# Optimization experiments

Measured on AMD Instinct MI355X. Metric: run time of the kernel, lower is better.

## Reference

```python
import jax, jax.numpy as jnp
import numpy as np
import math

# ---- module hyperparameters (from init_kwargs) ----
IN_CHANS, OUT_CHANS = 64, 64
NLAT_IN, NLON_IN = 91, 180
NLAT_OUT, NLON_OUT = 91, 180  # same resolution -> longitudinal stride 1
NR, NPHI = 5, 6               # kernel_shape
KSIZE = (NR - 1) * NPHI + 1   # 25 basis functions (1 center + (NR-1)*NPHI ring sectors)
THETA_CUTOFF = 4.0 * math.pi / float(NLAT_OUT - 1)
# latitude support window: basis vanishes for |theta_out - theta_in| > cutoff
_HALF = int(math.ceil(THETA_CUTOFF / (math.pi / (NLAT_IN - 1))))
WIN = 2 * _HALF + 1


def _precompute_psi():
    """Precompute DISCO basis tensor psi (values of the piecewise-linear
    spherical basis functions, weighted by quadrature weights), restricted to
    the latitudinal support window. Returns (psi [K,To,W,P], ti_idx [To,W])."""
    theta_in = np.pi * np.arange(NLAT_IN) / (NLAT_IN - 1)    # equiangular colatitudes
    theta_out = np.pi * np.arange(NLAT_OUT) / (NLAT_OUT - 1)
    phi_in = 2.0 * np.pi * np.arange(NLON_IN) / NLON_IN
    offs = np.arange(-_HALF, _HALF + 1)
    ti_raw = np.arange(NLAT_OUT)[:, None] + offs[None, :]    # [To, W]
    valid = (ti_raw >= 0) & (ti_raw < NLAT_IN)
    ti_idx = np.clip(ti_raw, 0, NLAT_IN - 1)
    to = theta_out[:, None, None]                            # [To,1,1]
    ti = theta_in[ti_idx][:, :, None]                        # [To,W,1]
    ph = phi_in[None, None, :]                               # [1,1,P]
    # coordinates of input point in frame where the output point (theta_out, 0)
    # is rotated to the north pole (rotation by -theta_out about y-axis)
    xx = np.cos(to) * np.sin(ti) * np.cos(ph) - np.sin(to) * np.cos(ti)
    yy = np.sin(ti) * np.sin(ph)
    zz = np.sin(to) * np.sin(ti) * np.cos(ph) + np.cos(to) * np.cos(ti)
    r = np.arccos(np.clip(zz, -1.0, 1.0))                    # great-circle distance
    phi = np.mod(np.arctan2(yy, xx), 2.0 * np.pi)            # azimuth around output point
    dr = THETA_CUTOFF / (NR - 1)
    dphi = 2.0 * np.pi / NPHI
    inside = (r <= THETA_CUTOFF) & valid[:, :, None]
    psi = np.zeros((KSIZE,) + r.shape, dtype=np.float64)
    # k = 0: isotropic center hat
    psi[0] = np.where(inside, np.maximum(0.0, 1.0 - r / dr), 0.0)
    # rings ir = 1..NR-1, azimuthal sectors ip = 0..NPHI-1 (periodic hat in phi)
    for ir in range(1, NR):
        rad = np.maximum(0.0, 1.0 - np.abs(r - ir * dr) / dr)
        for ip in range(NPHI):
            dp = np.abs(np.mod(phi - ip * dphi + np.pi, 2.0 * np.pi) - np.pi)
            ang = np.maximum(0.0, 1.0 - dp / dphi)
            psi[1 + (ir - 1) * NPHI + ip] = np.where(inside, rad * ang, 0.0)
    # fold in equiangular quadrature weights of the input grid
    quad = np.sin(theta_in) * (np.pi / (NLAT_IN - 1)) * (2.0 * np.pi / NLON_IN)
    psi = psi * quad[ti_idx][None, :, :, None]
    return jnp.asarray(psi, dtype=jnp.float32), jnp.asarray(ti_idx, dtype=jnp.int32)


PSI, TI_IDX = _precompute_psi()  # PSI: [K, To, W, P], TI_IDX: [To, W]


def setup_inputs() -> dict:
    key = jax.random.key(0)
    k1, k2 = jax.random.split(key)
    x = jax.random.normal(k1, (2, IN_CHANS, NLAT_IN, NLON_IN), dtype=jnp.float32)
    scale = 1.0 / math.sqrt(IN_CHANS * KSIZE)
    weight = scale * jax.random.normal(k2, (OUT_CHANS, IN_CHANS, KSIZE), dtype=jnp.float32)
    return {"x": x, "weight": weight}


def reference(x, weight):
    # DISCO S2 conv: out[b,o,to,q] = sum_{c,k} w[o,c,k] * sum_{ti,p} psi[k,to,ti,(p-q) mod P] * x[b,c,ti,p]
    # The longitudinal shift is a circular cross-correlation -> evaluate via rFFT.
    x = x.astype(jnp.float32)  # wrapper casts to float32 around the conv
    xw = x[:, :, TI_IDX, :]                          # [B,C,To,W,P] latitudinal gather
    Xf = jnp.fft.rfft(xw, axis=-1)                   # [B,C,To,W,F]
    Pf = jnp.fft.rfft(PSI, axis=-1)                  # [K,To,W,F]
    # correlation: FFT(z) = conj(FFT(psi)) * FFT(x), contracting the lat window
    Zf = jnp.einsum('ktwf,bctwf->bcktf', jnp.conj(Pf), Xf)   # [B,C,K,To,F]
    Of = jnp.einsum('ock,bcktf->botf', weight.astype(Zf.dtype), Zf)
    out = jnp.fft.irfft(Of, n=NLON_IN, axis=-1)      # [B,Cout,To,P]
    return out.astype(x.dtype)
```

## Files before the change

### kernel.cpp

```cpp
#include <hip/hip_runtime.h>
#include <math.h>
#include <string.h>

#define NLAT 91
#define NLON 180
#define NCH  64
#define KSZ  25
#define NW   9
#define HALF 4
#define NB   2
#define NP2  32
#define CGRP 16
#define PPB  2
#define THREADS 192
#define PCAP  49152
#define CCAP  2048

#define CLS_OFF   0
#define PSIS_OFF  11520
#define BLOB_MAX  (PSIS_OFF + (size_t)PCAP * 16 + 64 + (size_t)PCAP * 4)

#ifndef M_PI
#define M_PI 3.14159265358979323846
#endif

typedef unsigned int u32;

static int build_tables(unsigned char* blob, size_t* offs_off_out)
{
#pragma clang fp contract(off)
    int*   clsOff = (int*)(blob + CLS_OFF);
    float* psis   = (float*)(blob + PSIS_OFF);

    static double sth[NLAT], cth[NLAT], cphv[NLON], sphv[NLON];
    for (int t = 0; t < NLAT; t++) {
        double th = (M_PI * (double)t) / 90.0;
        sth[t] = sin(th); cth[t] = cos(th);
    }
    for (int q = 0; q < NLON; q++) {
        double ph = (2.0 * M_PI * (double)q) / 180.0;
        cphv[q] = cos(ph); sphv[q] = sin(ph);
    }
    const double cutoff = (4.0 * M_PI) / 90.0;
    const double dr     = cutoff / 4.0;
    const double dphi   = (2.0 * M_PI) / 6.0;

    static u32   coff[30][CCAP];
    static float cps[30][CCAP][4];
    static int   ccnt[30];
    static u32   toffs[PCAP];

    int np = 0;
    for (int t = 0; t < NLAT; t++) {
        for (int c = 0; c < 30; c++) ccnt[c] = 0;

        for (int w = 0; w < NW; w++) {
            int ti_raw = t - HALF + w;
            int valid = (ti_raw >= 0) && (ti_raw < NLAT);
            int ti = ti_raw < 0 ? 0 : (ti_raw > NLAT - 1 ? NLAT - 1 : ti_raw);
            for (int dq = -89; dq <= 90; dq++) {
                int q = dq < 0 ? dq + NLON : dq;
                double t1 = sth[t] * sth[ti];
                double t2 = t1 * cphv[q];
                double t3 = cth[t] * cth[ti];
                double zz = t2 + t3;
                if (zz > 1.0) zz = 1.0;
                if (zz < -1.0) zz = -1.0;
                double r = acos(zz);
                if (!(valid && (r <= cutoff))) continue;
                double xx = (cth[t] * sth[ti]) * cphv[q] - sth[t] * cth[ti];
                double yy = sth[ti] * sphv[q];
                double phi = atan2(yy, xx);
                { double m = fmod(phi, 2.0 * M_PI); if (m < 0.0) m += 2.0 * M_PI; phi = m; }
                double quad = sth[ti] * (M_PI / 90.0) * ((2.0 * M_PI) / 180.0);

                int ir = (int)floor(r / dr);  if (ir > 4) ir = 4; if (ir < 0) ir = 0;
                int ip = (int)floor(phi / dphi); if (ip > 5) ip = 5; if (ip < 0) ip = 0;
                int ip1 = (ip + 1) % 6;

                double angL, angH;
                {
                    double a = (phi - ip * dphi) + M_PI;
                    double m = fmod(a, 2.0 * M_PI); if (m < 0.0) m += 2.0 * M_PI;
                    double dp = fabs(m - M_PI);
                    angL = fmax(0.0, 1.0 - dp / dphi);
                }
                {
                    double a = (phi - ip1 * dphi) + M_PI;
                    double m = fmod(a, 2.0 * M_PI); if (m < 0.0) m += 2.0 * M_PI;
                    double dp = fabs(m - M_PI);
                    angH = fmax(0.0, 1.0 - dp / dphi);
                }
                float s0 = 0.f, s1 = 0.f, s2 = 0.f, s3 = 0.f;
                if (ir == 0) {
                    double rad0 = fmax(0.0, 1.0 - r / dr);
                    double rad1 = fmax(0.0, 1.0 - fabs(r - dr) / dr);
                    s0 = (float)(rad0 * quad);
                    s1 = (float)((rad1 * angL) * quad);
                    s2 = (float)((rad1 * angH) * quad);
                } else if (ir == 4) {
                    double rad4 = fmax(0.0, 1.0 - fabs(r - 4.0 * dr) / dr);
                    s0 = (float)((rad4 * angL) * quad);
                    s1 = (float)((rad4 * angH) * quad);
                } else {
                    double radL = fmax(0.0, 1.0 - fabs(r - ir * dr) / dr);
                    double radH = fmax(0.0, 1.0 - fabs(r - (ir + 1) * dr) / dr);
                    s0 = (float)((radL * angL) * quad);
                    s1 = (float)((radL * angH) * quad);
                    s2 = (float)((radH * angL) * quad);
                    s3 = (float)((radH * angH) * quad);
                }
                if (s0 == 0.f && s1 == 0.f && s2 == 0.f && s3 == 0.f) continue;
                int cls = ir * 6 + ip;
                int n = ccnt[cls];
                if (n < CCAP) {
                    coff[cls][n] = (u32)(ti * 360 + dq + 90);
                    cps[cls][n][0] = s0; cps[cls][n][1] = s1;
                    cps[cls][n][2] = s2; cps[cls][n][3] = s3;
                    ccnt[cls] = n + 1;
                }
            }
        }
        for (int cls = 0; cls < 30; cls++) {
            clsOff[t * 31 + cls] = np;
            for (int i = 0; i < ccnt[cls] && np < PCAP; i++) {
                toffs[np] = coff[cls][i];
                psis[4 * np + 0] = cps[cls][i][0];
                psis[4 * np + 1] = cps[cls][i][1];
                psis[4 * np + 2] = cps[cls][i][2];
                psis[4 * np + 3] = cps[cls][i][3];
                np++;
            }
        }
        clsOff[t * 31 + 30] = np;
    }
    size_t offs_off = (PSIS_OFF + (size_t)np * 16 + 63) & ~(size_t)63;
    memcpy(blob + offs_off, toffs, (size_t)np * 4);
    *offs_off_out = offs_off;
    return np;
}

struct GInit {
    unsigned char* blob;
    int np;
    size_t bytes, offs_off;
    GInit() {
        static unsigned char storage[BLOB_MAX];
        np = build_tables(storage, &offs_off);
        bytes = offs_off + (size_t)np * 4;
        unsigned char* p = nullptr;
        if (hipHostMalloc((void**)&p, bytes) == hipSuccess && p) {
            memcpy(p, storage, bytes);
            blob = p;
        } else {
            blob = storage;
        }
    }
};
static GInit g_init;

__global__ __launch_bounds__(THREADS) void pack_x2(const float* __restrict__ x,
                                                   float2* __restrict__ xd)
{
    int t = blockIdx.x, cp2 = blockIdx.y, b = blockIdx.z;
    const float* x0 = x + ((size_t)(b * NCH + cp2 * 2) * NLAT + t) * NLON;
    const float* x1 = x0 + (size_t)NLAT * NLON;
    float2* dst = xd + ((size_t)(b * NP2 + cp2) * NLAT + t) * 360;
    for (int u = threadIdx.x; u < 360; u += THREADS) {
        int s = u + 90;
        if (s >= NLON) s -= NLON;
        if (s >= NLON) s -= NLON;
        dst[u] = make_float2(x0[s], x1[s]);
    }
}

__global__ void pack_w2(const float* __restrict__ wgt, float2* __restrict__ wt2)
{
    int i = blockIdx.x * blockDim.x + threadIdx.x;
    if (i >= NP2 * KSZ * NCH) return;
    int cp2 = i / (KSZ * NCH);
    int rem = i - cp2 * (KSZ * NCH);
    int k = rem / NCH;
    int o = rem - k * NCH;
    float2 v;
    v.x = wgt[((size_t)o * NCH + cp2 * 2 + 0) * KSZ + k];
    v.y = wgt[((size_t)o * NCH + cp2 * 2 + 1) * KSZ + k];
    wt2[i] = v;
}

template<int ROW, int IP>
__device__ __forceinline__ void runSeg2(int sBeg, int sEnd,
    const u32* __restrict__ offsG, const float4* __restrict__ psisG,
    const float2* __restrict__ xgb, int p,
    float (&z0)[2], float (&zA)[6][2], float (&zB)[6][2])
{
    constexpr int IP1 = (IP + 1) % 6;
#pragma unroll 2
    for (int s = sBeg; s < sEnd; ++s) {
        u32 off = offsG[s];
        float4 ps = psisG[s];
        float2 xv = xgb[off + p];
        if (ROW == 0) {
            z0[0] = fmaf(ps.x, xv.x, z0[0]);  z0[1] = fmaf(ps.x, xv.y, z0[1]);
            zB[IP][0] = fmaf(ps.y, xv.x, zB[IP][0]);   zB[IP][1] = fmaf(ps.y, xv.y, zB[IP][1]);
            zB[IP1][0] = fmaf(ps.z, xv.x, zB[IP1][0]); zB[IP1][1] = fmaf(ps.z, xv.y, zB[IP1][1]);
        } else if (ROW == 4) {
            zA[IP][0] = fmaf(ps.x, xv.x, zA[IP][0]);   zA[IP][1] = fmaf(ps.x, xv.y, zA[IP][1]);
            zA[IP1][0] = fmaf(ps.y, xv.x, zA[IP1][0]); zA[IP1][1] = fmaf(ps.y, xv.y, zA[IP1][1]);
        } else {
            zA[IP][0] = fmaf(ps.x, xv.x, zA[IP][0]);   zA[IP][1] = fmaf(ps.x, xv.y, zA[IP][1]);
            zA[IP1][0] = fmaf(ps.y, xv.x, zA[IP1][0]); zA[IP1][1] = fmaf(ps.y, xv.y, zA[IP1][1]);
            zB[IP][0] = fmaf(ps.z, xv.x, zB[IP][0]);   zB[IP][1] = fmaf(ps.z, xv.y, zB[IP][1]);
            zB[IP1][0] = fmaf(ps.w, xv.x, zB[IP1][0]); zB[IP1][1] = fmaf(ps.w, xv.y, zB[IP1][1]);
        }
    }
}

__device__ __forceinline__ void flushRing2(float (&acc)[NCH],
    const float2* __restrict__ wt2cp, int kbase, const float (&zR)[6][2])
{
#pragma clang loop unroll(disable)
    for (int j = 0; j < 6; j++) {
        float zc0, zc1;
        switch (j) {
            case 0:  zc0 = zR[0][0]; zc1 = zR[0][1]; break;
            case 1:  zc0 = zR[1][0]; zc1 = zR[1][1]; break;
            case 2:  zc0 = zR[2][0]; zc1 = zR[2][1]; break;
            case 3:  zc0 = zR[3][0]; zc1 = zR[3][1]; break;
            case 4:  zc0 = zR[4][0]; zc1 = zR[4][1]; break;
            default: zc0 = zR[5][0]; zc1 = zR[5][1]; break;
        }
        const float2* wk = wt2cp + (size_t)(kbase + j) * NCH;
#pragma unroll
        for (int o = 0; o < NCH; o++) {
            float2 w2 = wk[o];
            acc[o] = fmaf(w2.y, zc1, fmaf(w2.x, zc0, acc[o]));
        }
    }
}

__global__ __launch_bounds__(THREADS, 4) void disco_fused(
    const float2* __restrict__ xg, const float2* __restrict__ wt2,
    const u32* __restrict__ offsG, const float4* __restrict__ psisG,
    const int* __restrict__ clsOffG, float* __restrict__ out)
{
    int t = blockIdx.x, cg = blockIdx.y, b = blockIdx.z;
    int tid = threadIdx.x;
    int p = tid < NLON ? tid : NLON - 1;
    bool act = tid < NLON;
    const int* co = clsOffG + t * 31;

    float acc[NCH];
#pragma unroll
    for (int o = 0; o < NCH; o++) acc[o] = 0.f;

#pragma clang loop unroll(disable)
    for (int pk = 0; pk < PPB; pk++) {
        int cp2 = cg * PPB + pk;
        const float2* xgb = xg + (size_t)(b * NP2 + cp2) * NLAT * 360;
        const float2* wt2cp = wt2 + (size_t)cp2 * KSZ * NCH;

        float z0[2] = {0.f, 0.f};
        float zA[6][2], zB[6][2];
#pragma unroll
        for (int j = 0; j < 6; j++) {
            zA[j][0] = 0.f; zA[j][1] = 0.f;
            zB[j][0] = 0.f; zB[j][1] = 0.f;
        }

#define SEG(ROW, IP) runSeg2<ROW, IP>(co[(ROW)*6+(IP)], co[(ROW)*6+(IP)+1], \
                                      offsG, psisG, xgb, p, z0, zA, zB)
#define ROW6(ROW) SEG(ROW,0); SEG(ROW,1); SEG(ROW,2); SEG(ROW,3); SEG(ROW,4); SEG(ROW,5)
#define ROLL() { _Pragma("unroll") for (int j = 0; j < 6; j++) { \
                   zA[j][0] = zB[j][0]; zB[j][0] = 0.f; \
                   zA[j][1] = zB[j][1]; zB[j][1] = 0.f; } }

        ROW6(0);
        {
            const float2* wk = wt2cp;
#pragma unroll
            for (int o = 0; o < NCH; o++) {
                float2 w2 = wk[o];
                acc[o] = fmaf(w2.y, z0[1], fmaf(w2.x, z0[0], acc[o]));
            }
        }
        ROLL();
        ROW6(1);
        flushRing2(acc, wt2cp, 1, zA);
        ROLL();
        ROW6(2);
        flushRing2(acc, wt2cp, 7, zA);
        ROLL();
        ROW6(3);
        flushRing2(acc, wt2cp, 13, zA);
        ROLL();
        ROW6(4);
        flushRing2(acc, wt2cp, 19, zA);
#undef SEG
#undef ROW6
#undef ROLL
    }

    if (act) {
        float* op = out + ((size_t)b * NCH * NLAT * NLON) + (size_t)t * NLON + p;
#pragma unroll
        for (int o = 0; o < NCH; o++)
            atomicAdd(op + (size_t)o * (NLAT * NLON), acc[o]);
    }
}

extern "C" void kernel_launch(void* const* d_in, const int* in_sizes, int n_in,
                              void* d_out, int out_size, void* d_ws, size_t ws_size,
                              hipStream_t stream)
{
    const float* x   = (const float*)d_in[0];
    const float* wgt = (const float*)d_in[1];
    char* ws = (char*)d_ws;

    size_t cur = 0;
    auto alloc = [&](size_t bytes) { size_t o = cur; cur = (cur + bytes + 255) & ~(size_t)255; return o; };
    size_t blob_off = alloc(BLOB_MAX);
    size_t xd2_off  = alloc((size_t)NB * NP2 * NLAT * 360 * 8);
    size_t wt2_off  = alloc((size_t)NP2 * KSZ * NCH * 8);

    unsigned char* d_blob = (unsigned char*)(ws + blob_off);
    float2*        xd2    = (float2*)(ws + xd2_off);
    float2*        wt2    = (float2*)(ws + wt2_off);

    hipMemcpyAsync(d_blob, g_init.blob, g_init.bytes, hipMemcpyHostToDevice, stream);
    pack_x2<<<dim3(NLAT, NP2, NB), THREADS, 0, stream>>>(x, xd2);
    pack_w2<<<(NP2 * KSZ * NCH + 255) / 256, 256, 0, stream>>>(wgt, wt2);
    hipMemsetAsync(d_out, 0, (size_t)out_size * 4, stream);

    const u32*    offsD = (const u32*)(d_blob + g_init.offs_off);
    const float4* psisD = (const float4*)(d_blob + PSIS_OFF);
    const int*    clsD  = (const int*)(d_blob + CLS_OFF);

    disco_fused<<<dim3(NLAT, CGRP, NB), THREADS, 0, stream>>>(
        xd2, wt2, offsD, psisD, clsD, (float*)d_out);
}
```

Measured before the change: 487.9 us.

## Split heavy latitude rows into balanced work blocks with LDS-staged tables

Builds a descriptor table on the host that splits each output latitude's sparse psi entries into chunks of roughly equal size, and launches one block per chunk instead of one per latitude, to even out load across blocks (rows near the poles carry many more entries). Each block copies its offsets and psi values into shared memory before the gather loop, which is unrolled further. Blocks that share a latitude now produce partial sums for the same outputs, which presumably relies on the existing flush accumulating atomically into the zeroed output. The cost is more blocks that redo the weight contraction, plus a shared-memory fill and a barrier.

Result: slower. 699.8 us (+43.4%).

```diff
diff --git a/kernel.cpp b/kernel.cpp
--- a/kernel.cpp
+++ b/kernel.cpp
@@ -13,11 +13,15 @@
 #define CGRP 16
 #define PPB  2
 #define THREADS 192
-#define PCAP  49152
+#define PCAP  32768
 #define CCAP  2048
-
-#define CLS_OFF   0
-#define PSIS_OFF  11520
+#define PTGT  224
+#define TCAP  288
+#define DCAP  256
+#define DLEN  40
+
+#define DESC_OFF  0
+#define PSIS_OFF  40960
 #define BLOB_MAX  (PSIS_OFF + (size_t)PCAP * 16 + 64 + (size_t)PCAP * 4)
 
 #ifndef M_PI
@@ -26,11 +30,11 @@
 
 typedef unsigned int u32;
 
-static int build_tables(unsigned char* blob, size_t* offs_off_out)
+static int build_tables(unsigned char* blob, size_t* offs_off_out, int* np_out)
 {
 #pragma clang fp contract(off)
-    int*   clsOff = (int*)(blob + CLS_OFF);
-    float* psis   = (float*)(blob + PSIS_OFF);
+    int*   desc = (int*)(blob + DESC_OFF);
+    float* psis = (float*)(blob + PSIS_OFF);
 
     static double sth[NLAT], cth[NLAT], cphv[NLON], sphv[NLON];
     for (int t = 0; t < NLAT; t++) {
@@ -48,12 +52,14 @@
     static u32   coff[30][CCAP];
     static float cps[30][CCAP][4];
     static int   ccnt[30];
-    static u32   toffs[PCAP];
+    static u32   soff[PCAP];
+    static float spsi[PCAP][4];
+    static int   clsOff[NLAT][31];
+    static u32   roff[PCAP];
 
     int np = 0;
     for (int t = 0; t < NLAT; t++) {
         for (int c = 0; c < 30; c++) ccnt[c] = 0;
-
         for (int w = 0; w < NW; w++) {
             int ti_raw = t - HALF + w;
             int valid = (ti_raw >= 0) && (ti_raw < NLAT);
@@ -122,31 +128,60 @@
             }
         }
         for (int cls = 0; cls < 30; cls++) {
-            clsOff[t * 31 + cls] = np;
+            clsOff[t][cls] = np;
             for (int i = 0; i < ccnt[cls] && np < PCAP; i++) {
-                toffs[np] = coff[cls][i];
-                psis[4 * np + 0] = cps[cls][i][0];
-                psis[4 * np + 1] = cps[cls][i][1];
-                psis[4 * np + 2] = cps[cls][i][2];
-                psis[4 * np + 3] = cps[cls][i][3];
+                soff[np] = coff[cls][i];
+                spsi[np][0] = cps[cls][i][0]; spsi[np][1] = cps[cls][i][1];
+                spsi[np][2] = cps[cls][i][2]; spsi[np][3] = cps[cls][i][3];
                 np++;
             }
         }
-        clsOff[t * 31 + 30] = np;
-    }
-    size_t offs_off = (PSIS_OFF + (size_t)np * 16 + 63) & ~(size_t)63;
-    memcpy(blob + offs_off, toffs, (size_t)np * 4);
+        clsOff[t][30] = np;
+    }
+
+    int nBlk = 0, pos = 0;
+    for (int t = 0; t < NLAT; t++) {
+        int np_t = clsOff[t][30] - clsOff[t][0];
+        int S = (np_t + PTGT - 1) / PTGT;
+        if (S < 1) S = 1;
+        for (int s = 0; s < S && nBlk < DCAP; s++) {
+            int* D = desc + nBlk * DLEN;
+            D[0] = t; D[1] = pos;
+            int loc = 0;
+            for (int j = 0; j < 30; j++) {
+                int beg = clsOff[t][j];
+                int len = clsOff[t][j + 1] - beg;
+                int lo = beg + (int)((long long)len * s / S);
+                int hi = beg + (int)((long long)len * (s + 1) / S);
+                D[8 + j] = loc;
+                for (int i = lo; i < hi; i++) {
+                    roff[pos] = soff[i];
+                    psis[4 * pos + 0] = spsi[i][0];
+                    psis[4 * pos + 1] = spsi[i][1];
+                    psis[4 * pos + 2] = spsi[i][2];
+                    psis[4 * pos + 3] = spsi[i][3];
+                    pos++; loc++;
+                }
+            }
+            D[8 + 30] = loc;
+            D[2] = loc;
+            nBlk++;
+        }
+    }
+    size_t offs_off = (PSIS_OFF + (size_t)pos * 16 + 63) & ~(size_t)63;
+    memcpy(blob + offs_off, roff, (size_t)pos * 4);
     *offs_off_out = offs_off;
-    return np;
+    *np_out = pos;
+    return nBlk;
 }
 
 struct GInit {
     unsigned char* blob;
-    int np;
+    int nBlk, np;
     size_t bytes, offs_off;
     GInit() {
         static unsigned char storage[BLOB_MAX];
-        np = build_tables(storage, &offs_off);
+        nBlk = build_tables(storage, &offs_off, &np);
         bytes = offs_off + (size_t)np * 4;
         unsigned char* p = nullptr;
         if (hipHostMalloc((void**)&p, bytes) == hipSuccess && p) {
@@ -189,16 +224,16 @@
 }
 
 template<int ROW, int IP>
-__device__ __forceinline__ void runSeg2(int sBeg, int sEnd,
-    const u32* __restrict__ offsG, const float4* __restrict__ psisG,
+__device__ __forceinline__ void runSegL(int iBeg, int iEnd,
+    const u32* sOff, const float4* sPsi,
     const float2* __restrict__ xgb, int p,
     float (&z0)[2], float (&zA)[6][2], float (&zB)[6][2])
 {
     constexpr int IP1 = (IP + 1) % 6;
-#pragma unroll 2
-    for (int s = sBeg; s < sEnd; ++s) {
-        u32 off = offsG[s];
-        float4 ps = psisG[s];
+#pragma unroll 4
+    for (int i = iBeg; i < iEnd; ++i) {
+        u32 off = sOff[i];
+        float4 ps = sPsi[i];
         float2 xv = xgb[off + p];
         if (ROW == 0) {
             z0[0] = fmaf(ps.x, xv.x, z0[0]);  z0[1] = fmaf(ps.x, xv.y, z0[1]);
@@ -241,14 +276,25 @@
 
 __global__ __launch_bounds__(THREADS, 4) void disco_fused(
     const float2* __restrict__ xg, const float2* __restrict__ wt2,
-    const u32* __restrict__ offsG, const float4* __restrict__ psisG,
-    const int* __restrict__ clsOffG, float* __restrict__ out)
-{
-    int t = blockIdx.x, cg = blockIdx.y, b = blockIdx.z;
+    const int* __restrict__ descG, const u32* __restrict__ offsG,
+    const float4* __restrict__ psisG, float* __restrict__ out)
+{
+    int blk = blockIdx.x, cg = blockIdx.y, b = blockIdx.z;
+    const int* D = descG + blk * DLEN;
+    int t    = __builtin_amdgcn_readfirstlane(D[0]);
+    int base = __builtin_amdgcn_readfirstlane(D[1]);
+    int cnt  = __builtin_amdgcn_readfirstlane(D[2]);
     int tid = threadIdx.x;
     int p = tid < NLON ? tid : NLON - 1;
     bool act = tid < NLON;
-    const int* co = clsOffG + t * 31;
+
+    __shared__ u32    sOff[TCAP];
+    __shared__ float4 sPsi[TCAP];
+    for (int i = tid; i < cnt; i += THREADS) {
+        sOff[i] = offsG[base + i];
+        sPsi[i] = psisG[base + i];
+    }
+    __syncthreads();
 
     float acc[NCH];
 #pragma unroll
@@ -268,8 +314,8 @@
             zB[j][0] = 0.f; zB[j][1] = 0.f;
         }
 
-#define SEG(ROW, IP) runSeg2<ROW, IP>(co[(ROW)*6+(IP)], co[(ROW)*6+(IP)+1], \
-                                      offsG, psisG, xgb, p, z0, zA, zB)
+#define SEG(ROW, IP) runSegL<ROW, IP>(D[8 + (ROW)*6 + (IP)], D[8 + (ROW)*6 + (IP) + 1], \
+                                      sOff, sPsi, xgb, p, z0, zA, zB)
 #define ROW6(ROW) SEG(ROW,0); SEG(ROW,1); SEG(ROW,2); SEG(ROW,3); SEG(ROW,4); SEG(ROW,5)
 #define ROLL() { _Pragma("unroll") for (int j = 0; j < 6; j++) { \
                    zA[j][0] = zB[j][0]; zB[j][0] = 0.f; \
@@ -332,10 +378,10 @@
     pack_w2<<<(NP2 * KSZ * NCH + 255) / 256, 256, 0, stream>>>(wgt, wt2);
     hipMemsetAsync(d_out, 0, (size_t)out_size * 4, stream);
 
+    const int*    descD = (const int*)(d_blob + DESC_OFF);
     const u32*    offsD = (const u32*)(d_blob + g_init.offs_off);
     const float4* psisD = (const float4*)(d_blob + PSIS_OFF);
-    const int*    clsD  = (const int*)(d_blob + CLS_OFF);
-
-    disco_fused<<<dim3(NLAT, CGRP, NB), THREADS, 0, stream>>>(
-        xd2, wt2, offsD, psisD, clsD, (float*)d_out);
-}
+
+    disco_fused<<<dim3(g_init.nBlk, CGRP, NB), THREADS, 0, stream>>>(
+        xd2, wt2, descD, offsD, psisD, (float*)d_out);
+}
```
